# Kernel tuning notes

Hardware: AMD Instinct MI355X
Metric: run time of the kernel (lower is better)

The kernel has to match this reference:

```python
import jax, jax.numpy as jnp
import numpy as np

B, S, IN_DIM, OUT_DIM = 4, 2048, 1024, 1024
NEG = -9e15

def _xavier(key, shape, gain=1.414):
    fan_in, fan_out = shape[0], shape[1]
    a = gain * np.sqrt(6.0 / (fan_in + fan_out))
    return jax.random.uniform(key, shape, jnp.float32, -a, a)

def setup_inputs() -> dict:
    key = jax.random.key(0)
    ks = jax.random.split(key, 8)
    x = jax.random.normal(ks[0], (B, S, IN_DIM), jnp.float32)
    W_query = _xavier(ks[1], (IN_DIM, OUT_DIM))
    W_key = _xavier(ks[2], (IN_DIM, OUT_DIM))
    W_value = _xavier(ks[3], (IN_DIM, OUT_DIM))
    # torch Linear default init (kaiming-uniform-ish); values don't matter for correctness baseline
    W1 = _xavier(ks[4], (OUT_DIM + IN_DIM, OUT_DIM), gain=1.0)
    b1 = jnp.zeros((OUT_DIM,), jnp.float32)
    W2 = _xavier(ks[5], (OUT_DIM, OUT_DIM), gain=1.0)
    b2 = jnp.zeros((OUT_DIM,), jnp.float32)
    return {"x": x, "W_query": W_query, "W_key": W_key, "W_value": W_value,
            "W1": W1, "b1": b1, "W2": W2, "b2": b2}

def reference(x, W_query, W_key, W_value, W1, b1, W2, b2):
    # QKV projections: [B,S,in] @ [in,out] -> [B,S,out]
    q = jnp.einsum('bsi,io->bso', x, W_query)
    k = jnp.einsum('bsi,io->bso', x, W_key)
    v = jnp.einsum('bsi,io->bso', x, W_value)
    scale = 1.0 / jnp.sqrt(jnp.float32(OUT_DIM))
    e = jnp.einsum('bqd,bkd->bqk', q, k) * scale  # [B,S,S]
    causal = jnp.tril(jnp.ones((S, S), jnp.float32))  # mask > 0 keeps lower triangle
    attn = jnp.where(causal > 0, e, jnp.float32(NEG))
    attn = jax.nn.softmax(attn, axis=2)
    # dropout: eval mode (train=False) -> identity
    out = jnp.einsum('bqk,bkd->bqd', attn, v)  # [B,S,out]
    h = jnp.concatenate([out, x], axis=-1)  # [B,S,out+in]
    h = jax.nn.relu(jnp.einsum('bsf,fo->bso', h, W1) + b1)
    return jnp.einsum('bsf,fo->bso', h, W2) + b2
```

## Files before the change

kernel.cpp:

```cpp
#include <hip/hip_runtime.h>
#include <stdint.h>

typedef __attribute__((ext_vector_type(8))) short short8;
typedef __attribute__((ext_vector_type(4))) float f32x4;

__device__ __forceinline__ unsigned short f32_to_bf16(float f) {
    unsigned int u = __float_as_uint(f);
    u += 0x7FFFu + ((u >> 16) & 1u);
    return (unsigned short)(u >> 16);
}

__device__ __forceinline__ short8 load8_f32_as_bf16(const float* __restrict__ ap) {
    f32x4 f0 = *(const f32x4*)ap;
    f32x4 f1 = *(const f32x4*)(ap + 4);
    union { short8 s; unsigned short u[8]; } cv;
#pragma unroll
    for (int t = 0; t < 4; ++t) {
        cv.u[t]     = f32_to_bf16(f0[t]);
        cv.u[t + 4] = f32_to_bf16(f1[t]);
    }
    return cv.s;
}

__device__ __forceinline__ void gld_lds16(const void* g, void* l) {
    __builtin_amdgcn_global_load_lds(
        (const __attribute__((address_space(1))) unsigned int*)(unsigned long long)(uintptr_t)g,
        (__attribute__((address_space(3))) unsigned int*)(unsigned int)(uintptr_t)l,
        16, 0, 0);
}

__device__ __forceinline__ int triC(int y) {
    int t = y >> 1;
    return y + t * (t - 1) + ((y & 1) ? t : 0);
}

template<int AMODE, int EPI, int SWIZ, bool KLIMIT, int MT>
__global__ __launch_bounds__(256, 4)
void gemm128(const unsigned short* __restrict__ A, const unsigned short* __restrict__ A2,
             int lda, int lda2, int ksplit,
             const unsigned short* __restrict__ B, int ldb,
             void* __restrict__ C, int ldc, int K,
             long aStride, long bStride, long cStride,
             const float* __restrict__ bias, long biasStride, float scale,
             void* __restrict__ C2, int ldc2)
{
    int z = blockIdx.z;
    int mblk, nblk;
    if (SWIZ == 1) {
        int lin = blockIdx.y * gridDim.x + blockIdx.x;
        int mchunk = gridDim.y >> 3;
        int xcd = lin & 7, idx = lin >> 3;
        mblk = xcd * mchunk + idx % mchunk;
        nblk = idx / mchunk;
    } else if (SWIZ == 4) {
        mblk = (z & 2) ? ((int)gridDim.y - 1 - (int)blockIdx.y) : blockIdx.y;
        nblk = blockIdx.x;
    } else if (SWIZ == 5) {
        int x = blockIdx.x;
        int a = (int)(2.f * sqrtf((float)x));
        if (a > 31) a = 31;
        while (a < 31 && triC(a + 1) <= x) ++a;
        while (a > 0 && triC(a) > x) --a;
        mblk = a;
        nblk = x - triC(a);
    } else if (SWIZ == 6) {
        int x = blockIdx.x, yy = blockIdx.y;
        if (z < 2) { mblk = x * 8 + (yy & 7); nblk = yy >> 3; }
        else       { nblk = x * 8 + (yy & 7); mblk = yy >> 3; }
    } else {
        mblk = blockIdx.y;
        nblk = blockIdx.x;
    }
    int m0 = mblk * MT;
    int n0 = nblk * 128;

    const unsigned short* Ab;
    const unsigned short* Bb;
    if (SWIZ == 6) {
        if (z < 2) { Ab = A; Bb = B + (size_t)z * bStride; }
        else       { Ab = B + (size_t)2 * bStride; Bb = A; }
    } else {
        Ab = A + (size_t)z * aStride;
        Bb = B + (size_t)z * bStride;
    }

    __shared__ __align__(16) short As[MT * 64];
    __shared__ __align__(16) short Bs[128 * 64];

    int tid  = threadIdx.x;
    int lane = tid & 63, wid = tid >> 6;
    constexpr int MI = MT / 32;
    int wm = (wid & 1) * (MT / 2), wn = (wid >> 1) * 64;
    int fr = lane & 15, fq = lane >> 4;
    int sw0 = ((fq    ) ^ (fr & 7)) * 16;
    int sw1 = ((fq ^ 4) ^ (fr & 7)) * 16;

    int rS = tid >> 3;
    int cS = ((tid & 7) ^ (rS & 7)) * 8;
    char* AsB = (char*)As; char* BsB = (char*)Bs;

    int kend = KLIMIT ? min(K, m0 + MT) : K;

    f32x4 acc[MI][4];
#pragma unroll
    for (int i = 0; i < MI; ++i)
#pragma unroll
    for (int j = 0; j < 4; ++j) acc[i][j] = f32x4{0.f, 0.f, 0.f, 0.f};

    for (int k0 = 0; k0 < kend; k0 += 64) {
        const unsigned short* Asrc = Ab;
        int koff = k0, ldax = lda;
        if (AMODE == 2 && k0 >= ksplit) { Asrc = A2; koff = k0 - ksplit; ldax = lda2; }
        const unsigned short* pa = Asrc + (size_t)(m0 + rS) * ldax + koff + cS;
        const unsigned short* pb = Bb   + (size_t)(n0 + rS) * ldb  + k0   + cS;
#pragma unroll
        for (int t = 0; t < MT / 32; ++t)
            gld_lds16(pa + (size_t)(32 * t) * ldax, AsB + t * 4096 + tid * 16);
#pragma unroll
        for (int t = 0; t < 4; ++t)
            gld_lds16(pb + (size_t)(32 * t) * ldb,  BsB + t * 4096 + tid * 16);
        __syncthreads();

#pragma unroll
        for (int kh = 0; kh < 2; ++kh) {
            int sw = kh ? sw1 : sw0;
            short8 a[MI], b[4];
#pragma unroll
            for (int i = 0; i < MI; ++i)
                a[i] = *(const short8*)(AsB + (wm + i * 16 + fr) * 128 + sw);
#pragma unroll
            for (int j = 0; j < 4; ++j)
                b[j] = *(const short8*)(BsB + (wn + j * 16 + fr) * 128 + sw);
#pragma unroll
            for (int i = 0; i < MI; ++i)
#pragma unroll
            for (int j = 0; j < 4; ++j)
                acc[i][j] = __builtin_amdgcn_mfma_f32_16x16x32_bf16(a[i], b[j], acc[i][j], 0, 0, 0);
        }
        __syncthreads();
    }

    if (EPI == 0) {
        unsigned short* Cz; int ldcz;
        if (SWIZ == 6 && z >= 2) { Cz = (unsigned short*)C2; ldcz = ldc2; }
        else { Cz = (unsigned short*)C + (size_t)z * cStride; ldcz = ldc; }
#pragma unroll
        for (int i = 0; i < MI; ++i)
#pragma unroll
        for (int j = 0; j < 4; ++j)
#pragma unroll
        for (int r = 0; r < 4; ++r) {
            int row = m0 + wm + i * 16 + fq * 4 + r;
            int col = n0 + wn + j * 16 + fr;
            Cz[(size_t)row * ldcz + col] = f32_to_bf16(acc[i][j][r]);
        }
    } else if (EPI == 6) {
        unsigned short* Cz = (unsigned short*)C + (size_t)z * cStride;
        float* rs = const_cast<float*>(bias) + z * biasStride;
#pragma unroll
        for (int i = 0; i < MI; ++i)
#pragma unroll
        for (int r = 0; r < 4; ++r) {
            int row = m0 + wm + i * 16 + fq * 4 + r;
            float s = 0.f;
#pragma unroll
            for (int j = 0; j < 4; ++j) {
                int col = n0 + wn + j * 16 + fr;
                float e = (col <= row) ? __expf(acc[i][j][r] * scale - 16.f) : 0.f;
                s += e;
                Cz[(size_t)row * ldc + col] = f32_to_bf16(e);
            }
            s += __shfl_xor(s, 1);
            s += __shfl_xor(s, 2);
            s += __shfl_xor(s, 4);
            s += __shfl_xor(s, 8);
            if (fr == 0) atomicAdd(&rs[row], s);
        }
    } else if (EPI == 4) {
        unsigned short* Cz = (unsigned short*)C + (size_t)z * cStride;
#pragma unroll
        for (int i = 0; i < MI; ++i)
#pragma unroll
        for (int r = 0; r < 4; ++r) {
            int row = m0 + wm + i * 16 + fq * 4 + r;
            float inv = 1.f / bias[z * biasStride + row];
#pragma unroll
            for (int j = 0; j < 4; ++j) {
                int col = n0 + wn + j * 16 + fr;
                Cz[(size_t)row * ldc + col] = f32_to_bf16(acc[i][j][r] * inv);
            }
        }
    } else {
#pragma unroll
        for (int i = 0; i < MI; ++i)
#pragma unroll
        for (int j = 0; j < 4; ++j)
#pragma unroll
        for (int r = 0; r < 4; ++r) {
            int row = m0 + wm + i * 16 + fq * 4 + r;
            int col = n0 + wn + j * 16 + fr;
            float v = acc[i][j][r];
            if (EPI == 2) {
                v += bias[col];
                v = v > 0.f ? v : 0.f;
                ((unsigned short*)C + (size_t)z * cStride)[(size_t)row * ldc + col] = f32_to_bf16(v);
            } else {
                ((float*)C + (size_t)z * cStride)[(size_t)row * ldc + col] = v + bias[col];
            }
        }
    }
}

template<int AMODE, int EPI, int SWIZ>
__global__ __launch_bounds__(512, 2)
void gemm8p(const unsigned short* __restrict__ A, const unsigned short* __restrict__ A2,
            int lda, int lda2, int ksplit,
            const unsigned short* __restrict__ B, int ldb,
            void* __restrict__ C, int ldc, int K,
            long bStride, long cStride,
            const float* __restrict__ bias,
            void* __restrict__ C2, int ldc2)
{
    constexpr int BM = 256, BN = 128;
    int z = blockIdx.z;
    int lin = blockIdx.y * gridDim.x + blockIdx.x;
    int xcd = lin & 7, idx = lin >> 3;
    int mblk, nblk;
    if (SWIZ == 6) {
        if (z < 2) { mblk = xcd * 4 + (idx & 3); nblk = idx >> 2; }
        else       { nblk = xcd * 8 + (idx & 7); mblk = idx >> 3; }
    } else {
        int mch = (int)gridDim.y >> 3;
        mblk = xcd * mch + idx % mch;
        nblk = idx / mch;
    }
    int m0 = mblk * BM, n0 = nblk * BN;

    const unsigned short *Ab, *Bb;
    if (SWIZ == 6) {
        if (z < 2) { Ab = A; Bb = B + (size_t)z * bStride; }
        else       { Ab = B + (size_t)2 * bStride; Bb = A; }
    } else { Ab = A; Bb = B; }

    constexpr int ATILE = BM * 64;
    constexpr int BTILE = BN * 64;
    constexpr int TILE  = ATILE + BTILE;
    __shared__ __align__(16) short lds[3 * TILE];

    int tid  = threadIdx.x;
    int lane = tid & 63, wid = tid >> 6;
    int wm = (wid & 3) * 64, wn = (wid >> 2) * 64;
    int fr = lane & 15, fq = lane >> 4;
    int sw0 = ((fq    ) ^ (fr & 7)) * 16;
    int sw1 = ((fq ^ 4) ^ (fr & 7)) * 16;

    int rS = tid >> 3;
    int cS = ((tid & 7) ^ (rS & 7)) * 8;

    int NT = K >> 6;

    f32x4 acc[4][4];
#pragma unroll
    for (int i = 0; i < 4; ++i)
#pragma unroll
    for (int j = 0; j < 4; ++j) acc[i][j] = f32x4{0.f, 0.f, 0.f, 0.f};

    auto STAGE = [&](int t, int slot) {
        int k0 = t << 6;
        char* dst = (char*)(lds + slot * TILE);
        const unsigned short* Asrc = Ab; int koff = k0, ldax = lda;
        if (AMODE == 2 && k0 >= ksplit) { Asrc = A2; koff = k0 - ksplit; ldax = lda2; }
        const unsigned short* pa = Asrc + (size_t)(m0 + rS) * ldax + koff + cS;
        const unsigned short* pb = Bb   + (size_t)(n0 + rS) * ldb  + k0   + cS;
#pragma unroll
        for (int u = 0; u < 4; ++u)
            gld_lds16(pa + (size_t)(64 * u) * ldax, dst + u * 8192 + tid * 16);
#pragma unroll
        for (int u = 0; u < 2; ++u)
            gld_lds16(pb + (size_t)(64 * u) * ldb, dst + 32768 + u * 8192 + tid * 16);
    };

    STAGE(0, 0);
    STAGE(1, 1);
    asm volatile("s_waitcnt vmcnt(6)" ::: "memory");
    __builtin_amdgcn_s_barrier();
    __builtin_amdgcn_sched_barrier(0);
    asm volatile("" ::: "memory");

    int sc = 0, ss = 2;
    for (int t = 0; t < NT; ++t) {
        if (t + 2 < NT) STAGE(t + 2, ss);
        const char* AsB = (const char*)(lds + sc * TILE);
        const char* BsB = AsB + 32768;
#pragma unroll
        for (int kh = 0; kh < 2; ++kh) {
            int sw = kh ? sw1 : sw0;
            short8 a[4], b[4];
#pragma unroll
            for (int i = 0; i < 4; ++i)
                a[i] = *(const short8*)(AsB + (wm + i * 16 + fr) * 128 + sw);
#pragma unroll
            for (int j = 0; j < 4; ++j)
                b[j] = *(const short8*)(BsB + (wn + j * 16 + fr) * 128 + sw);
            __builtin_amdgcn_s_setprio(1);
#pragma unroll
            for (int i = 0; i < 4; ++i)
#pragma unroll
            for (int j = 0; j < 4; ++j)
                acc[i][j] = __builtin_amdgcn_mfma_f32_16x16x32_bf16(a[i], b[j], acc[i][j], 0, 0, 0);
            __builtin_amdgcn_s_setprio(0);
        }
        if (t + 1 < NT) {
            if (t + 2 < NT) { asm volatile("s_waitcnt vmcnt(6)" ::: "memory"); }
            else            { asm volatile("s_waitcnt vmcnt(0)" ::: "memory"); }
            __builtin_amdgcn_s_barrier();
            __builtin_amdgcn_sched_barrier(0);
            asm volatile("" ::: "memory");
        }
        sc = sc == 2 ? 0 : sc + 1;
        ss = ss == 2 ? 0 : ss + 1;
    }

    if (EPI == 0) {
        unsigned short* Cz; int ldcz;
        if (SWIZ == 6 && z >= 2) { Cz = (unsigned short*)C2; ldcz = ldc2; }
        else { Cz = (unsigned short*)C + (size_t)z * cStride; ldcz = ldc; }
#pragma unroll
        for (int i = 0; i < 4; ++i)
#pragma unroll
        for (int j = 0; j < 4; ++j)
#pragma unroll
        for (int r = 0; r < 4; ++r) {
            int row = m0 + wm + i * 16 + fq * 4 + r;
            int col = n0 + wn + j * 16 + fr;
            Cz[(size_t)row * ldcz + col] = f32_to_bf16(acc[i][j][r]);
        }
    } else if (EPI == 2) {
        unsigned short* Cz = (unsigned short*)C;
#pragma unroll
        for (int i = 0; i < 4; ++i)
#pragma unroll
        for (int j = 0; j < 4; ++j)
#pragma unroll
        for (int r = 0; r < 4; ++r) {
            int row = m0 + wm + i * 16 + fq * 4 + r;
            int col = n0 + wn + j * 16 + fr;
            float v = acc[i][j][r] + bias[col];
            v = v > 0.f ? v : 0.f;
            Cz[(size_t)row * ldc + col] = f32_to_bf16(v);
        }
    } else {
        float* Cz = (float*)C;
#pragma unroll
        for (int i = 0; i < 4; ++i)
#pragma unroll
        for (int j = 0; j < 4; ++j)
#pragma unroll
        for (int r = 0; r < 4; ++r) {
            int row = m0 + wm + i * 16 + fq * 4 + r;
            int col = n0 + wn + j * 16 + fr;
            Cz[(size_t)row * ldc + col] = acc[i][j][r] + bias[col];
        }
    }
}

__device__ __forceinline__ void transpose_tile32(const float* __restrict__ in,
                                                 unsigned short* __restrict__ out,
                                                 int rows, int cols, int bx, int by, int tid)
{
    __shared__ float t[32][33];
    int tx = tid & 31, ty = tid >> 5;
    int r0 = by * 32, c0 = bx * 32;
#pragma unroll
    for (int i = 0; i < 4; ++i)
        t[ty + i * 8][tx] = in[(size_t)(r0 + ty + i * 8) * cols + c0 + tx];
    __syncthreads();
#pragma unroll
    for (int i = 0; i < 4; ++i)
        out[(size_t)(c0 + ty + i * 8) * rows + r0 + tx] = f32_to_bf16(t[tx][ty + i * 8]);
}

__global__ __launch_bounds__(256)
void prep_kernel(const float* __restrict__ x,
                 const float* __restrict__ Wq, const float* __restrict__ Wk,
                 const float* __restrict__ Wv, const float* __restrict__ W1,
                 const float* __restrict__ W2,
                 unsigned short* __restrict__ xb, unsigned short* __restrict__ WT,
                 unsigned short* __restrict__ W1T, unsigned short* __restrict__ W2T,
                 float* __restrict__ rsum)
{
    int idx = blockIdx.x;
    int tid = threadIdx.x;
    if (idx < 4096) {
        size_t i = ((size_t)idx * 256 + tid) * 8;
        *(short8*)(xb + i) = load8_f32_as_bf16(x + i);
    } else if (idx < 7168) {
        int t = idx - 4096;
        int w = t >> 10; t &= 1023;
        const float* in = w == 0 ? Wq : (w == 1 ? Wk : Wv);
        transpose_tile32(in, WT + (size_t)w * 1024 * 1024, 1024, 1024,
                         t & 31, t >> 5, tid);
    } else if (idx < 9216) {
        int t = idx - 7168;
        transpose_tile32(W1, W1T, 2048, 1024, t & 31, t >> 5, tid);
    } else if (idx < 10240) {
        int t = idx - 9216;
        transpose_tile32(W2, W2T, 1024, 1024, t & 31, t >> 5, tid);
    } else {
        int t = idx - 10240;
        f32x4 zero = {0.f, 0.f, 0.f, 0.f};
        float* p = rsum + ((size_t)t * 256 + tid) * 8;
        *(f32x4*)p = zero;
        *(f32x4*)(p + 4) = zero;
    }
}

extern "C" void kernel_launch(void* const* d_in, const int* in_sizes, int n_in,
                              void* d_out, int out_size, void* d_ws, size_t ws_size,
                              hipStream_t stream)
{
    const float* x  = (const float*)d_in[0];
    const float* Wq = (const float*)d_in[1];
    const float* Wk = (const float*)d_in[2];
    const float* Wv = (const float*)d_in[3];
    const float* W1 = (const float*)d_in[4];
    const float* b1 = (const float*)d_in[5];
    const float* W2 = (const float*)d_in[6];
    const float* b2 = (const float*)d_in[7];
    float* out = (float*)d_out;

    size_t off = 0;
    auto alloc = [&](size_t bytes) {
        char* r = (char*)d_ws + off;
        off += (bytes + 255) & ~(size_t)255;
        return r;
    };
    const size_t TOK = (size_t)8192 * 1024;
    unsigned short* WT   = (unsigned short*)alloc((size_t)3072 * 1024 * 2);
    unsigned short* W1T  = (unsigned short*)alloc((size_t)1024 * 2048 * 2);
    unsigned short* W2T  = (unsigned short*)alloc((size_t)1024 * 1024 * 2);
    unsigned short* xb   = (unsigned short*)alloc(TOK * 2);
    unsigned short* vT   = (unsigned short*)alloc((size_t)1024 * 8192 * 2);
    unsigned short* attn = (unsigned short*)alloc(TOK * 2);
    float*          rsum = (float*)         alloc((size_t)4 * 2048 * 4);
    unsigned short* q    = (unsigned short*)alloc(TOK * 2);
    unsigned short* k    = (unsigned short*)alloc(TOK * 2);
    unsigned short* S    = (unsigned short*)alloc((size_t)4 * 2048 * 2048 * 2);
    unsigned short* h1   = S;

    prep_kernel<<<10244, 256, 0, stream>>>(x, Wq, Wk, Wv, W1, W2, xb, WT, W1T, W2T, rsum);

    gemm8p<0, 0, 6><<<dim3(4, 64, 3), 512, 0, stream>>>(
        xb, nullptr, 1024, 0, 0, WT, 1024, q, 1024, 1024,
        (long)1024 * 1024, (long)TOK, nullptr, vT, 8192);

    gemm128<0, 6, 5, false, 64><<<dim3(272, 1, 4), 256, 0, stream>>>(
        q, nullptr, 1024, 0, 0, k, 1024, S, 2048, 1024,
        (long)2048 * 1024, (long)2048 * 1024, (long)2048 * 2048, rsum, 2048, 0.03125f,
        nullptr, 0);
    gemm128<0, 4, 4, true, 64><<<dim3(8, 32, 4), 256, 0, stream>>>(
        S, nullptr, 2048, 0, 0, vT, 8192, attn, 1024, 2048,
        (long)2048 * 2048, (long)2048, (long)2048 * 1024, rsum, 2048, 0.f, nullptr, 0);

    gemm8p<2, 2, 1><<<dim3(8, 32, 1), 512, 0, stream>>>(
        attn, xb, 1024, 1024, 1024, W1T, 2048, h1, 1024, 2048,
        0, 0, b1, nullptr, 0);
    gemm8p<0, 3, 1><<<dim3(8, 32, 1), 512, 0, stream>>>(
        h1, nullptr, 1024, 0, 0, W2T, 1024, out, 1024, 1024,
        0, 0, b2, nullptr, 0);
}
```

Measured before the change: 291.0 us.

## Rework big GEMM into half-K double-buffered pipeline and split QKV launch

Replaces the 256x128 GEMM's three-slot LDS ring of 64-wide K tiles with a scheme that stages each K tile as two 32-wide halves in two alternating buffers. It interleaves LDS reads, the next global-to-LDS copies and MFMA blocks, with a different swizzle and finer waits. The fused QKV launch, which used z-dependent operand swapping for V, is split into a batched Q/K launch and a separate V-transposed launch with its own XCD swizzle. Dead SWIZ==6 and epilogue code is removed from the 128-tile kernel. The aim is better overlap of memory loads with MFMA, at the cost of more barriers and an extra launch.

```diff
diff --git a/kernel.cpp b/kernel.cpp
--- a/kernel.cpp
+++ b/kernel.cpp
@@ -63,10 +63,6 @@
         while (a > 0 && triC(a) > x) --a;
         mblk = a;
         nblk = x - triC(a);
-    } else if (SWIZ == 6) {
-        int x = blockIdx.x, yy = blockIdx.y;
-        if (z < 2) { mblk = x * 8 + (yy & 7); nblk = yy >> 3; }
-        else       { nblk = x * 8 + (yy & 7); mblk = yy >> 3; }
     } else {
         mblk = blockIdx.y;
         nblk = blockIdx.x;
@@ -74,15 +70,8 @@
     int m0 = mblk * MT;
     int n0 = nblk * 128;
 
-    const unsigned short* Ab;
-    const unsigned short* Bb;
-    if (SWIZ == 6) {
-        if (z < 2) { Ab = A; Bb = B + (size_t)z * bStride; }
-        else       { Ab = B + (size_t)2 * bStride; Bb = A; }
-    } else {
-        Ab = A + (size_t)z * aStride;
-        Bb = B + (size_t)z * bStride;
-    }
+    const unsigned short* Ab = A + (size_t)z * aStride;
+    const unsigned short* Bb = B + (size_t)z * bStride;
 
     __shared__ __align__(16) short As[MT * 64];
     __shared__ __align__(16) short Bs[128 * 64];
@@ -140,21 +129,7 @@
         __syncthreads();
     }
 
-    if (EPI == 0) {
-        unsigned short* Cz; int ldcz;
-        if (SWIZ == 6 && z >= 2) { Cz = (unsigned short*)C2; ldcz = ldc2; }
-        else { Cz = (unsigned short*)C + (size_t)z * cStride; ldcz = ldc; }
-#pragma unroll
-        for (int i = 0; i < MI; ++i)
-#pragma unroll
-        for (int j = 0; j < 4; ++j)
-#pragma unroll
-        for (int r = 0; r < 4; ++r) {
-            int row = m0 + wm + i * 16 + fq * 4 + r;
-            int col = n0 + wn + j * 16 + fr;
-            Cz[(size_t)row * ldcz + col] = f32_to_bf16(acc[i][j][r]);
-        }
-    } else if (EPI == 6) {
+    if (EPI == 6) {
         unsigned short* Cz = (unsigned short*)C + (size_t)z * cStride;
         float* rs = const_cast<float*>(bias) + z * biasStride;
 #pragma unroll
@@ -191,6 +166,7 @@
             }
         }
     } else {
+        unsigned short* Cz = (unsigned short*)C + (size_t)z * cStride;
 #pragma unroll
         for (int i = 0; i < MI; ++i)
 #pragma unroll
@@ -199,63 +175,47 @@
         for (int r = 0; r < 4; ++r) {
             int row = m0 + wm + i * 16 + fq * 4 + r;
             int col = n0 + wn + j * 16 + fr;
-            float v = acc[i][j][r];
-            if (EPI == 2) {
-                v += bias[col];
-                v = v > 0.f ? v : 0.f;
-                ((unsigned short*)C + (size_t)z * cStride)[(size_t)row * ldc + col] = f32_to_bf16(v);
-            } else {
-                ((float*)C + (size_t)z * cStride)[(size_t)row * ldc + col] = v + bias[col];
-            }
+            Cz[(size_t)row * ldc + col] = f32_to_bf16(acc[i][j][r]);
         }
     }
 }
 
 template<int AMODE, int EPI, int SWIZ>
 __global__ __launch_bounds__(512, 2)
-void gemm8p(const unsigned short* __restrict__ A, const unsigned short* __restrict__ A2,
+void gemm2p(const unsigned short* __restrict__ A, const unsigned short* __restrict__ A2,
             int lda, int lda2, int ksplit,
             const unsigned short* __restrict__ B, int ldb,
             void* __restrict__ C, int ldc, int K,
             long bStride, long cStride,
-            const float* __restrict__ bias,
-            void* __restrict__ C2, int ldc2)
+            const float* __restrict__ bias)
 {
-    constexpr int BM = 256, BN = 128;
     int z = blockIdx.z;
     int lin = blockIdx.y * gridDim.x + blockIdx.x;
     int xcd = lin & 7, idx = lin >> 3;
     int mblk, nblk;
-    if (SWIZ == 6) {
-        if (z < 2) { mblk = xcd * 4 + (idx & 3); nblk = idx >> 2; }
-        else       { nblk = xcd * 8 + (idx & 7); mblk = idx >> 3; }
+    if (SWIZ == 2) {
+        int nch = (int)gridDim.x >> 3;
+        nblk = xcd * nch + idx % nch;
+        mblk = idx / nch;
     } else {
         int mch = (int)gridDim.y >> 3;
         mblk = xcd * mch + idx % mch;
         nblk = idx / mch;
     }
-    int m0 = mblk * BM, n0 = nblk * BN;
-
-    const unsigned short *Ab, *Bb;
-    if (SWIZ == 6) {
-        if (z < 2) { Ab = A; Bb = B + (size_t)z * bStride; }
-        else       { Ab = B + (size_t)2 * bStride; Bb = A; }
-    } else { Ab = A; Bb = B; }
-
-    constexpr int ATILE = BM * 64;
-    constexpr int BTILE = BN * 64;
-    constexpr int TILE  = ATILE + BTILE;
-    __shared__ __align__(16) short lds[3 * TILE];
+    int m0 = mblk * 256, n0 = nblk * 128;
+
+    const unsigned short* Bb = B + (size_t)z * bStride;
+
+    __shared__ __align__(16) char lds[98304];
 
     int tid  = threadIdx.x;
     int lane = tid & 63, wid = tid >> 6;
     int wm = (wid & 3) * 64, wn = (wid >> 2) * 64;
     int fr = lane & 15, fq = lane >> 4;
-    int sw0 = ((fq    ) ^ (fr & 7)) * 16;
-    int sw1 = ((fq ^ 4) ^ (fr & 7)) * 16;
-
-    int rS = tid >> 3;
-    int cS = ((tid & 7) ^ (rS & 7)) * 8;
+    int swA = (fq ^ ((fr >> 1) & 3)) * 16;
+
+    int rS  = tid >> 2;
+    int cSw = ((tid & 3) ^ ((tid >> 3) & 3)) * 8;
 
     int NT = K >> 6;
 
@@ -265,66 +225,82 @@
 #pragma unroll
     for (int j = 0; j < 4; ++j) acc[i][j] = f32x4{0.f, 0.f, 0.f, 0.f};
 
-    auto STAGE = [&](int t, int slot) {
-        int k0 = t << 6;
-        char* dst = (char*)(lds + slot * TILE);
-        const unsigned short* Asrc = Ab; int koff = k0, ldax = lda;
-        if (AMODE == 2 && k0 >= ksplit) { Asrc = A2; koff = k0 - ksplit; ldax = lda2; }
-        const unsigned short* pa = Asrc + (size_t)(m0 + rS) * ldax + koff + cS;
-        const unsigned short* pb = Bb   + (size_t)(n0 + rS) * ldb  + k0   + cS;
-#pragma unroll
-        for (int u = 0; u < 4; ++u)
-            gld_lds16(pa + (size_t)(64 * u) * ldax, dst + u * 8192 + tid * 16);
-#pragma unroll
-        for (int u = 0; u < 2; ++u)
-            gld_lds16(pb + (size_t)(64 * u) * ldb, dst + 32768 + u * 8192 + tid * 16);
+    auto STAGE_A = [&](int kt, int s) {
+        if (kt >= NT) return;
+        char* dst = lds + (((kt & 1) * 2 + s) * 16384) + tid * 16;
+        const unsigned short* Asrc = A; int koff = kt << 6; int ldax = lda;
+        if (AMODE == 2 && koff >= ksplit) { Asrc = A2; koff -= ksplit; ldax = lda2; }
+        const unsigned short* pa = Asrc + (size_t)(m0 + rS) * ldax + koff + (s << 5) + cSw;
+        gld_lds16(pa, dst);
+        gld_lds16(pa + (size_t)128 * ldax, dst + 8192);
     };
-
-    STAGE(0, 0);
-    STAGE(1, 1);
+    auto STAGE_B = [&](int kt, int s) {
+        if (kt >= NT) return;
+        char* dst = lds + 65536 + (((kt & 1) * 2 + s) * 8192) + tid * 16;
+        const unsigned short* pb = Bb + (size_t)(n0 + rS) * ldb + (kt << 6) + (s << 5) + cSw;
+        gld_lds16(pb, dst);
+    };
+
+    const char* Abase = lds + (wm + fr) * 64 + swA;
+    const char* Bbase = lds + 65536 + (wn + fr) * 64 + swA;
+
+    STAGE_A(0, 0); STAGE_B(0, 0);
+    STAGE_A(0, 1); STAGE_B(0, 1);
+    STAGE_A(1, 0); STAGE_B(1, 0);
     asm volatile("s_waitcnt vmcnt(6)" ::: "memory");
     __builtin_amdgcn_s_barrier();
+    asm volatile("" ::: "memory");
     __builtin_amdgcn_sched_barrier(0);
-    asm volatile("" ::: "memory");
-
-    int sc = 0, ss = 2;
+
     for (int t = 0; t < NT; ++t) {
-        if (t + 2 < NT) STAGE(t + 2, ss);
-        const char* AsB = (const char*)(lds + sc * TILE);
-        const char* BsB = AsB + 32768;
-#pragma unroll
-        for (int kh = 0; kh < 2; ++kh) {
-            int sw = kh ? sw1 : sw0;
-            short8 a[4], b[4];
-#pragma unroll
-            for (int i = 0; i < 4; ++i)
-                a[i] = *(const short8*)(AsB + (wm + i * 16 + fr) * 128 + sw);
-#pragma unroll
-            for (int j = 0; j < 4; ++j)
-                b[j] = *(const short8*)(BsB + (wn + j * 16 + fr) * 128 + sw);
-            __builtin_amdgcn_s_setprio(1);
-#pragma unroll
-            for (int i = 0; i < 4; ++i)
-#pragma unroll
-            for (int j = 0; j < 4; ++j)
-                acc[i][j] = __builtin_amdgcn_mfma_f32_16x16x32_bf16(a[i], b[j], acc[i][j], 0, 0, 0);
-            __builtin_amdgcn_s_setprio(0);
-        }
-        if (t + 1 < NT) {
-            if (t + 2 < NT) { asm volatile("s_waitcnt vmcnt(6)" ::: "memory"); }
-            else            { asm volatile("s_waitcnt vmcnt(0)" ::: "memory"); }
+        int d2 = (t & 1) * 2;
+        short8 a[4], b[4];
+#pragma unroll
+        for (int i = 0; i < 4; ++i) a[i] = *(const short8*)(Abase + (d2 + 0) * 16384 + i * 1024);
+#pragma unroll
+        for (int j = 0; j < 4; ++j) b[j] = *(const short8*)(Bbase + (d2 + 0) * 8192 + j * 1024);
+        STAGE_A(t + 1, 1); STAGE_B(t + 1, 1);
+        __builtin_amdgcn_s_barrier();
+        asm volatile("s_waitcnt lgkmcnt(0)" ::: "memory");
+        __builtin_amdgcn_sched_barrier(0);
+        __builtin_amdgcn_s_setprio(1);
+#pragma unroll
+        for (int i = 0; i < 4; ++i)
+#pragma unroll
+        for (int j = 0; j < 4; ++j)
+            acc[i][j] = __builtin_amdgcn_mfma_f32_16x16x32_bf16(a[i], b[j], acc[i][j], 0, 0, 0);
+        __builtin_amdgcn_s_setprio(0);
+        if (t == NT - 1) { asm volatile("s_waitcnt vmcnt(0)" ::: "memory"); }
+        else             { asm volatile("s_waitcnt vmcnt(6)" ::: "memory"); }
+        __builtin_amdgcn_s_barrier();
+        asm volatile("" ::: "memory");
+        __builtin_amdgcn_sched_barrier(0);
+#pragma unroll
+        for (int i = 0; i < 4; ++i) a[i] = *(const short8*)(Abase + (d2 + 1) * 16384 + i * 1024);
+#pragma unroll
+        for (int j = 0; j < 4; ++j) b[j] = *(const short8*)(Bbase + (d2 + 1) * 8192 + j * 1024);
+        STAGE_A(t + 2, 0); STAGE_B(t + 2, 0);
+        __builtin_amdgcn_s_barrier();
+        asm volatile("s_waitcnt lgkmcnt(0)" ::: "memory");
+        __builtin_amdgcn_sched_barrier(0);
+        __builtin_amdgcn_s_setprio(1);
+#pragma unroll
+        for (int i = 0; i < 4; ++i)
+#pragma unroll
+        for (int j = 0; j < 4; ++j)
+            acc[i][j] = __builtin_amdgcn_mfma_f32_16x16x32_bf16(a[i], b[j], acc[i][j], 0, 0, 0);
+        __builtin_amdgcn_s_setprio(0);
+        if (t < NT - 1) {
+            if (t == NT - 2) { asm volatile("s_waitcnt vmcnt(3)" ::: "memory"); }
+            else             { asm volatile("s_waitcnt vmcnt(6)" ::: "memory"); }
             __builtin_amdgcn_s_barrier();
+            asm volatile("" ::: "memory");
             __builtin_amdgcn_sched_barrier(0);
-            asm volatile("" ::: "memory");
-        }
-        sc = sc == 2 ? 0 : sc + 1;
-        ss = ss == 2 ? 0 : ss + 1;
+        }
     }
 
     if (EPI == 0) {
-        unsigned short* Cz; int ldcz;
-        if (SWIZ == 6 && z >= 2) { Cz = (unsigned short*)C2; ldcz = ldc2; }
-        else { Cz = (unsigned short*)C + (size_t)z * cStride; ldcz = ldc; }
+        unsigned short* Cz = (unsigned short*)C + (size_t)z * cStride;
 #pragma unroll
         for (int i = 0; i < 4; ++i)
 #pragma unroll
@@ -333,7 +309,7 @@
         for (int r = 0; r < 4; ++r) {
             int row = m0 + wm + i * 16 + fq * 4 + r;
             int col = n0 + wn + j * 16 + fr;
-            Cz[(size_t)row * ldcz + col] = f32_to_bf16(acc[i][j][r]);
+            Cz[(size_t)row * ldc + col] = f32_to_bf16(acc[i][j][r]);
         }
     } else if (EPI == 2) {
         unsigned short* Cz = (unsigned short*)C;
@@ -450,9 +426,13 @@
 
     prep_kernel<<<10244, 256, 0, stream>>>(x, Wq, Wk, Wv, W1, W2, xb, WT, W1T, W2T, rsum);
 
-    gemm8p<0, 0, 6><<<dim3(4, 64, 3), 512, 0, stream>>>(
+    gemm2p<0, 0, 1><<<dim3(8, 32, 2), 512, 0, stream>>>(
         xb, nullptr, 1024, 0, 0, WT, 1024, q, 1024, 1024,
-        (long)1024 * 1024, (long)TOK, nullptr, vT, 8192);
+        (long)1024 * 1024, (long)TOK, nullptr);
+
+    gemm2p<0, 0, 2><<<dim3(64, 4, 1), 512, 0, stream>>>(
+        WT + (size_t)2 * 1024 * 1024, nullptr, 1024, 0, 0, xb, 1024,
+        vT, 8192, 1024, 0, 0, nullptr);
 
     gemm128<0, 6, 5, false, 64><<<dim3(272, 1, 4), 256, 0, stream>>>(
         q, nullptr, 1024, 0, 0, k, 1024, S, 2048, 1024,
@@ -462,10 +442,10 @@
         S, nullptr, 2048, 0, 0, vT, 8192, attn, 1024, 2048,
         (long)2048 * 2048, (long)2048, (long)2048 * 1024, rsum, 2048, 0.f, nullptr, 0);
 
-    gemm8p<2, 2, 1><<<dim3(8, 32, 1), 512, 0, stream>>>(
+    gemm2p<2, 2, 1><<<dim3(8, 32, 1), 512, 0, stream>>>(
         attn, xb, 1024, 1024, 1024, W1T, 2048, h1, 1024, 2048,
-        0, 0, b1, nullptr, 0);
-    gemm8p<0, 3, 1><<<dim3(8, 32, 1), 512, 0, stream>>>(
+        0, 0, b1);
+    gemm2p<0, 3, 1><<<dim3(8, 32, 1), 512, 0, stream>>>(
         h1, nullptr, 1024, 0, 0, W2T, 1024, out, 1024, 1024,
-        0, 0, b2, nullptr, 0);
-}
+        0, 0, b2);
+}
```

Result: slower. 304.9 us (+4.8%).
